# Kernel optimization log

Measured on AMD Instinct MI355X. Metric: run time of the kernel, lower is better.

The kernel has to match this reference:

```python
import jax, jax.numpy as jnp
import numpy as np

N = 100000   # nodes
E = 1600000  # edges (avg degree 16)
F = 128      # num_features
H = 128      # hidden_channels
C = 8        # num_classes


def _gcn_conv(x, src, dst, W, b, num_nodes):
    """PyG GCNConv: add self-loops, symmetric normalization, linear-then-aggregate, +bias."""
    h = x @ W  # [N, out]
    loops = jnp.arange(num_nodes, dtype=src.dtype)
    s = jnp.concatenate([src, loops])
    d = jnp.concatenate([dst, loops])
    deg = jax.ops.segment_sum(jnp.ones_like(s, dtype=h.dtype), d, num_segments=num_nodes)
    dinv = jax.lax.rsqrt(jnp.maximum(deg, 1.0))  # deg >= 1 thanks to self-loops
    norm = dinv[s] * dinv[d]  # [E+N]
    out = jax.ops.segment_sum(h[s] * norm[:, None], d, num_segments=num_nodes)
    return out + b


def setup_inputs() -> dict:
    key = jax.random.key(0)
    k1, k2, k3, k4 = jax.random.split(key, 4)
    x = jax.random.normal(k1, (N, F), dtype=jnp.float32)
    edge_index = jax.random.randint(k2, (2, E), 0, N, dtype=jnp.int32)
    W1 = jax.random.normal(k3, (F, H), dtype=jnp.float32) * (1.0 / np.sqrt(F))
    b1 = jnp.zeros((H,), dtype=jnp.float32)
    W2 = jax.random.normal(k4, (H, C), dtype=jnp.float32) * (1.0 / np.sqrt(H))
    b2 = jnp.zeros((C,), dtype=jnp.float32)
    return {"x": x, "edge_index": edge_index, "W1": W1, "b1": b1, "W2": W2, "b2": b2}


def reference(x, edge_index, W1, b1, W2, b2):
    src, dst = edge_index[0], edge_index[1]
    h = _gcn_conv(x, src, dst, W1, b1, N)
    h = jax.nn.relu(h)
    out = _gcn_conv(h, src, dst, W2, b2, N)
    return out
```

## Files before the change

kernel.cpp:

```cpp
#include <hip/hip_runtime.h>
#include <hip/hip_bf16.h>
#include <hip/hip_fp16.h>

#define NN 100000
#define EE 1600000
#define FF 128
#define HH 128
#define CC 8

#define CH 4096
#define NBK ((NN + 255) / 256)
#define NCH ((EE + CH - 1) / CH)
#define HSZ (NBK * NCH)

typedef _Float16 half8 __attribute__((ext_vector_type(8)));
typedef float f32x4 __attribute__((ext_vector_type(4)));

__global__ __launch_bounds__(1024) void k_scan1(const int* __restrict__ in,
                                                int* __restrict__ outp,
                                                int* __restrict__ bsum, int n) {
  __shared__ int sh[1024];
  int t = threadIdx.x;
  int i = blockIdx.x * 1024 + t;
  int v = (i < n) ? in[i] : 0;
  sh[t] = v;
  __syncthreads();
  for (int offs = 1; offs < 1024; offs <<= 1) {
    int add = (t >= offs) ? sh[t - offs] : 0;
    __syncthreads();
    sh[t] += add;
    __syncthreads();
  }
  if (i < n) outp[i] = sh[t] - v;
  if (t == 1023) bsum[blockIdx.x] = sh[1023];
}

__global__ __launch_bounds__(256) void k_scan2(int* __restrict__ bsum, int nb) {
  __shared__ int sh[256];
  int t = threadIdx.x;
  int v = (t < nb) ? bsum[t] : 0;
  sh[t] = v;
  __syncthreads();
  for (int offs = 1; offs < 256; offs <<= 1) {
    int add = (t >= offs) ? sh[t - offs] : 0;
    __syncthreads();
    sh[t] += add;
    __syncthreads();
  }
  if (t < nb) bsum[t] = sh[t] - v;
}

__global__ __launch_bounds__(1024) void k_scan3(int* __restrict__ outp,
                                                const int* __restrict__ bsum,
                                                int n, int e) {
  int i = blockIdx.x * 1024 + threadIdx.x;
  if (i < n) outp[i] += bsum[blockIdx.x];
  if (i == 0) outp[n] = e;
}

__global__ __launch_bounds__(256) void k_histA(const int* __restrict__ dst,
                                               int* __restrict__ hist) {
  __shared__ int lh[NBK];
  int c = blockIdx.x, t = threadIdx.x;
  for (int b = t; b < NBK; b += 256) lh[b] = 0;
  __syncthreads();
  int e0 = c * CH, e1 = min(e0 + CH, EE);
  for (int j = e0 + t; j < e1; j += 256) atomicAdd(&lh[dst[j] >> 8], 1);
  __syncthreads();
  for (int b = t; b < NBK; b += 256) hist[b * NCH + c] = lh[b];
}

__global__ __launch_bounds__(256) void k_scat_gemm1(
    const int* __restrict__ src, const int* __restrict__ dst,
    const int* __restrict__ hoff, unsigned int* __restrict__ stage,
    const float* __restrict__ x, const float* __restrict__ W,
    __half* __restrict__ h, int n) {
  __shared__ _Float16 Wl[128 * 128];
  int t = threadIdx.x;

  if (blockIdx.x < NCH) {
    int* lcur = (int*)Wl;
    int c = blockIdx.x;
    for (int b = t; b < NBK; b += 256) lcur[b] = hoff[b * NCH + c];
    __syncthreads();
    int e0 = c * CH, e1 = min(e0 + CH, EE);
    for (int j = e0 + t; j < e1; j += 256) {
      int d = dst[j];
      int pos = atomicAdd(&lcur[d >> 8], 1);
      stage[pos] = (unsigned int)src[j] | ((unsigned int)(d & 255) << 17);
    }
    return;
  }

  {
    int c = t & 127;
    int kg0 = t >> 7;
    for (int kg = kg0; kg < 16; kg += 2) {
      _Float16 tmp[8];
#pragma unroll
      for (int j = 0; j < 8; ++j)
        tmp[j] = (_Float16)W[(size_t)(kg * 8 + j) * 128 + c];
      int byteoff = (c * 256 + kg * 16) ^ ((c & 7) << 4);
      *(half8*)((char*)Wl + byteoff) = *(half8*)tmp;
    }
  }
  __syncthreads();

  int row0 = (blockIdx.x - NCH) * 64;
  int w = t >> 6, l = t & 63;
  int rw = w >> 1, cw = w & 1;
  int lr = l & 15, g = l >> 4;

  f32x4 acc[2][4];
#pragma unroll
  for (int ar = 0; ar < 2; ++ar)
#pragma unroll
    for (int bt = 0; bt < 4; ++bt)
#pragma unroll
      for (int r = 0; r < 4; ++r) acc[ar][bt][r] = 0.f;

  for (int kt = 0; kt < 4; ++kt) {
    half8 a[2];
#pragma unroll
    for (int ar = 0; ar < 2; ++ar) {
      int row = row0 + rw * 32 + ar * 16 + lr;
      if (row < n) {
        const float* p = &x[(size_t)row * 128 + kt * 32 + g * 8];
        float4 v0 = *(const float4*)p;
        float4 v1 = *(const float4*)(p + 4);
        a[ar][0] = (_Float16)v0.x; a[ar][1] = (_Float16)v0.y;
        a[ar][2] = (_Float16)v0.z; a[ar][3] = (_Float16)v0.w;
        a[ar][4] = (_Float16)v1.x; a[ar][5] = (_Float16)v1.y;
        a[ar][6] = (_Float16)v1.z; a[ar][7] = (_Float16)v1.w;
      } else {
#pragma unroll
        for (int j = 0; j < 8; ++j) a[ar][j] = (_Float16)0.f;
      }
    }
#pragma unroll
    for (int bt = 0; bt < 4; ++bt) {
      int c = cw * 64 + bt * 16 + lr;
      int byteoff = (c * 256 + kt * 64 + g * 16) ^ ((c & 7) << 4);
      half8 bb = *(const half8*)((const char*)Wl + byteoff);
      acc[0][bt] = __builtin_amdgcn_mfma_f32_16x16x32_f16(a[0], bb, acc[0][bt], 0, 0, 0);
      acc[1][bt] = __builtin_amdgcn_mfma_f32_16x16x32_f16(a[1], bb, acc[1][bt], 0, 0, 0);
    }
  }

#pragma unroll
  for (int ar = 0; ar < 2; ++ar)
#pragma unroll
    for (int bt = 0; bt < 4; ++bt)
#pragma unroll
      for (int r = 0; r < 4; ++r) {
        int row = row0 + rw * 32 + ar * 16 + g * 4 + r;
        int c = cw * 64 + bt * 16 + lr;
        if (row < n) h[(size_t)row * 128 + c] = __float2half(acc[ar][bt][r]);
      }
}

__global__ __launch_bounds__(256) void k_bucketB(const unsigned int* __restrict__ stage,
                                                 const int* __restrict__ hoff,
                                                 int* __restrict__ col,
                                                 int* __restrict__ rowptr,
                                                 float* __restrict__ dinv) {
  __shared__ int lcnt[256];
  __shared__ int lpart[256];
  int b = blockIdx.x, t = threadIdx.x;
  int n0 = b * 256;
  lcnt[t] = 0;
  __syncthreads();
  int e0 = hoff[b * NCH];
  int e1 = hoff[(b + 1) * NCH];
  for (int j = e0 + t; j < e1; j += 256)
    atomicAdd(&lcnt[stage[j] >> 17], 1);
  __syncthreads();
  int c = lcnt[t];
  lpart[t] = c;
  __syncthreads();
  for (int offs = 1; offs < 256; offs <<= 1) {
    int add = (t >= offs) ? lpart[t - offs] : 0;
    __syncthreads();
    lpart[t] += add;
    __syncthreads();
  }
  int base = e0 + lpart[t] - c;
  int node = n0 + t;
  if (node <= NN) rowptr[node] = base;
  if (node < NN) dinv[node] = rsqrtf((float)c + 1.f);
  __syncthreads();
  lcnt[t] = base;
  __syncthreads();
  for (int j = e0 + t; j < e1; j += 256) {
    unsigned int v = stage[j];
    int pos = atomicAdd(&lcnt[v >> 17], 1);
    col[pos] = (int)(v & 0x1FFFFu);
  }
}

__global__ __launch_bounds__(256) void k_agg1(const __half* __restrict__ h,
                                              const int* __restrict__ rowptr,
                                              const int* __restrict__ col,
                                              const float* __restrict__ dinv,
                                              const float* __restrict__ b1,
                                              __half2* __restrict__ out, int n) {
  int wid = threadIdx.x >> 6;
  int lane = threadIdx.x & 63;
  int node = blockIdx.x * 4 + wid;
  if (node >= n) return;
  float dn = dinv[node];
  const __half2* hp = (const __half2*)h;
  float2 acc = make_float2(0.f, 0.f);
  int e0 = rowptr[node], e1 = rowptr[node + 1];
  int e = e0;
  for (; e + 7 < e1; e += 8) {
    int s[8];
#pragma unroll
    for (int u = 0; u < 8; ++u) s[u] = col[e + u];
    float w[8];
    __half2 f[8];
#pragma unroll
    for (int u = 0; u < 8; ++u) w[u] = dinv[s[u]];
#pragma unroll
    for (int u = 0; u < 8; ++u) f[u] = hp[(size_t)s[u] * 64 + lane];
#pragma unroll
    for (int u = 0; u < 8; ++u) {
      float2 ff = __half22float2(f[u]);
      float ww = w[u] * dn;
      acc.x = fmaf(ww, ff.x, acc.x);
      acc.y = fmaf(ww, ff.y, acc.y);
    }
  }
  for (; e + 1 < e1; e += 2) {
    int s0 = col[e], s1 = col[e + 1];
    float w0 = dinv[s0] * dn, w1 = dinv[s1] * dn;
    float2 f0 = __half22float2(hp[(size_t)s0 * 64 + lane]);
    float2 f1 = __half22float2(hp[(size_t)s1 * 64 + lane]);
    acc.x = fmaf(w0, f0.x, acc.x); acc.y = fmaf(w0, f0.y, acc.y);
    acc.x = fmaf(w1, f1.x, acc.x); acc.y = fmaf(w1, f1.y, acc.y);
  }
  if (e < e1) {
    int s = col[e];
    float w = dinv[s] * dn;
    float2 f = __half22float2(hp[(size_t)s * 64 + lane]);
    acc.x = fmaf(w, f.x, acc.x);
    acc.y = fmaf(w, f.y, acc.y);
  }
  {
    float w = dn * dn;
    float2 f = __half22float2(hp[(size_t)node * 64 + lane]);
    acc.x = fmaf(w, f.x, acc.x);
    acc.y = fmaf(w, f.y, acc.y);
  }
  float2 bb = ((const float2*)b1)[lane];
  acc.x = fmaxf(acc.x + bb.x, 0.f);
  acc.y = fmaxf(acc.y + bb.y, 0.f);
  out[(size_t)node * 64 + lane] = __floats2half2_rn(acc.x, acc.y);
}

__global__ __launch_bounds__(256) void k_gemm2(const __half* __restrict__ a,
                                               const float* __restrict__ W2,
                                               __half* __restrict__ h2, int n) {
  int r = blockIdx.x * 256 + threadIdx.x;
  if (r >= n) return;
  float acc[8];
#pragma unroll
  for (int c = 0; c < 8; ++c) acc[c] = 0.f;
  const __half2* ap = (const __half2*)(a + (size_t)r * 128);
#pragma unroll 8
  for (int k2 = 0; k2 < 64; ++k2) {
    float2 v = __half22float2(ap[k2]);
    int k = k2 * 2;
#pragma unroll
    for (int c = 0; c < 8; ++c) {
      acc[c] = fmaf(v.x, W2[(k + 0) * 8 + c], acc[c]);
      acc[c] = fmaf(v.y, W2[(k + 1) * 8 + c], acc[c]);
    }
  }
  union { __half2 h2v[4]; uint4 u; } pk;
#pragma unroll
  for (int c = 0; c < 4; ++c)
    pk.h2v[c] = __floats2half2_rn(acc[2 * c], acc[2 * c + 1]);
  *(uint4*)&h2[(size_t)r * 8] = pk.u;
}

__global__ __launch_bounds__(256) void k_agg2(const __half* __restrict__ h2,
                                              const int* __restrict__ rowptr,
                                              const int* __restrict__ col,
                                              const float* __restrict__ dinv,
                                              const float* __restrict__ b2,
                                              float* __restrict__ out, int n) {
  int gthread = blockIdx.x * 256 + threadIdx.x;
  int node = gthread >> 3, f = gthread & 7;
  if (node >= n) return;
  float dn = dinv[node];
  float acc = 0.f;
  int e0 = rowptr[node], e1 = rowptr[node + 1];
  int e = e0;
  for (; e + 3 < e1; e += 4) {
    int s0 = col[e], s1 = col[e + 1], s2 = col[e + 2], s3 = col[e + 3];
    float w0 = dinv[s0], w1 = dinv[s1], w2 = dinv[s2], w3 = dinv[s3];
    float v0 = __half2float(h2[(size_t)s0 * 8 + f]);
    float v1 = __half2float(h2[(size_t)s1 * 8 + f]);
    float v2 = __half2float(h2[(size_t)s2 * 8 + f]);
    float v3 = __half2float(h2[(size_t)s3 * 8 + f]);
    acc = fmaf(w0 * dn, v0, acc);
    acc = fmaf(w1 * dn, v1, acc);
    acc = fmaf(w2 * dn, v2, acc);
    acc = fmaf(w3 * dn, v3, acc);
  }
  for (; e < e1; ++e) {
    int s = col[e];
    acc = fmaf(dinv[s] * dn, __half2float(h2[(size_t)s * 8 + f]), acc);
  }
  acc = fmaf(dn * dn, __half2float(h2[(size_t)node * 8 + f]), acc);
  out[(size_t)node * 8 + f] = acc + b2[f];
}

extern "C" void kernel_launch(void* const* d_in, const int* in_sizes, int n_in,
                              void* d_out, int out_size, void* d_ws, size_t ws_size,
                              hipStream_t stream) {
  const float* x  = (const float*)d_in[0];
  const int* eidx = (const int*)d_in[1];
  const float* W1 = (const float*)d_in[2];
  const float* b1 = (const float*)d_in[3];
  const float* W2 = (const float*)d_in[4];
  const float* b2 = (const float*)d_in[5];
  float* out = (float*)d_out;
  const int* src = eidx;
  const int* dst = eidx + EE;

  char* ws = (char*)d_ws;
  size_t off = 0;
  auto alloc = [&](size_t bytes) -> char* {
    char* p = ws + off;
    off = (off + bytes + 255) & ~(size_t)255;
    return p;
  };

  float*        dinv   = (float*)       alloc((size_t)NN * 4);
  int*          rowptr = (int*)         alloc((size_t)(NN + 1) * 4);
  int*          bsum   = (int*)         alloc(1024 * 4);
  int*          hist_g = (int*)         alloc((size_t)HSZ * 4);
  int*          hist_s = (int*)         alloc((size_t)(HSZ + 1) * 4);
  unsigned int* stage  = (unsigned int*)alloc((size_t)EE * 4);
  int*          colbuf = (int*)         alloc((size_t)EE * 4);
  __half*       h1     = (__half*)      alloc((size_t)NN * HH * 2);
  __half2*      agg1   = (__half2*)     alloc((size_t)NN * HH * 2);
  __half*       h2     = (__half*)h1;

  int nbScanH = (HSZ + 1023) / 1024;

  k_histA<<<NCH, 256, 0, stream>>>(dst, hist_g);
  k_scan1<<<nbScanH, 1024, 0, stream>>>(hist_g, hist_s, bsum, HSZ);
  k_scan2<<<1, 256, 0, stream>>>(bsum, nbScanH);
  k_scan3<<<nbScanH, 1024, 0, stream>>>(hist_s, bsum, HSZ, EE);

  int nbG1 = (NN + 63) / 64;
  k_scat_gemm1<<<NCH + nbG1, 256, 0, stream>>>(src, dst, hist_s, stage,
                                               x, W1, h1, NN);
  k_bucketB<<<NBK, 256, 0, stream>>>(stage, hist_s, colbuf, rowptr, dinv);

  k_agg1<<<(NN + 3) / 4, 256, 0, stream>>>(h1, rowptr, colbuf, dinv, b1, agg1, NN);
  k_gemm2<<<(NN + 255) / 256, 256, 0, stream>>>((const __half*)agg1, W2, h2, NN);
  k_agg2<<<(NN * 8 + 255) / 256, 256, 0, stream>>>(h2, rowptr, colbuf, dinv,
                                                   b2, out, NN);
}
```

Measured before the change: 165.9 us.

## Fuse second linear layer into aggregation and fold scan offsets into consumers

Merges the layer-2 matmul into the layer-1 aggregation kernel. Each wave stages its aggregated row in shared memory and reduces against W2 with cross-lane shuffles, so the 128-wide intermediate is never written to or re-read from global memory. The scan-add kernel is removed: consumers add the block sums on the fly. The histogram chunk size is doubled to shrink the histogram and scan, and the layer-2 gather loop is unrolled to 8. This removes two launches and a large intermediate buffer, at the cost of some extra shared-memory work and lower parallelism in the scatter phase.

```diff
diff --git a/kernel.cpp b/kernel.cpp
--- a/kernel.cpp
+++ b/kernel.cpp
@@ -8,7 +8,7 @@
 #define HH 128
 #define CC 8
 
-#define CH 4096
+#define CH 8192
 #define NBK ((NN + 255) / 256)
 #define NCH ((EE + CH - 1) / CH)
 #define HSZ (NBK * NCH)
@@ -50,14 +50,6 @@
   if (t < nb) bsum[t] = sh[t] - v;
 }
 
-__global__ __launch_bounds__(1024) void k_scan3(int* __restrict__ outp,
-                                                const int* __restrict__ bsum,
-                                                int n, int e) {
-  int i = blockIdx.x * 1024 + threadIdx.x;
-  if (i < n) outp[i] += bsum[blockIdx.x];
-  if (i == 0) outp[n] = e;
-}
-
 __global__ __launch_bounds__(256) void k_histA(const int* __restrict__ dst,
                                                int* __restrict__ hist) {
   __shared__ int lh[NBK];
@@ -72,7 +64,8 @@
 
 __global__ __launch_bounds__(256) void k_scat_gemm1(
     const int* __restrict__ src, const int* __restrict__ dst,
-    const int* __restrict__ hoff, unsigned int* __restrict__ stage,
+    const int* __restrict__ hist_s, const int* __restrict__ bsum,
+    unsigned int* __restrict__ stage,
     const float* __restrict__ x, const float* __restrict__ W,
     __half* __restrict__ h, int n) {
   __shared__ _Float16 Wl[128 * 128];
@@ -81,7 +74,10 @@
   if (blockIdx.x < NCH) {
     int* lcur = (int*)Wl;
     int c = blockIdx.x;
-    for (int b = t; b < NBK; b += 256) lcur[b] = hoff[b * NCH + c];
+    for (int b = t; b < NBK; b += 256) {
+      int idx = b * NCH + c;
+      lcur[b] = hist_s[idx] + bsum[idx >> 10];
+    }
     __syncthreads();
     int e0 = c * CH, e1 = min(e0 + CH, EE);
     for (int j = e0 + t; j < e1; j += 256) {
@@ -160,7 +156,8 @@
 }
 
 __global__ __launch_bounds__(256) void k_bucketB(const unsigned int* __restrict__ stage,
-                                                 const int* __restrict__ hoff,
+                                                 const int* __restrict__ hist_s,
+                                                 const int* __restrict__ bsum,
                                                  int* __restrict__ col,
                                                  int* __restrict__ rowptr,
                                                  float* __restrict__ dinv) {
@@ -169,9 +166,16 @@
   int b = blockIdx.x, t = threadIdx.x;
   int n0 = b * 256;
   lcnt[t] = 0;
-  __syncthreads();
-  int e0 = hoff[b * NCH];
-  int e1 = hoff[(b + 1) * NCH];
+  int i0 = b * NCH;
+  int e0 = hist_s[i0] + bsum[i0 >> 10];
+  int e1;
+  if (b == NBK - 1) {
+    e1 = EE;
+  } else {
+    int i1 = (b + 1) * NCH;
+    e1 = hist_s[i1] + bsum[i1 >> 10];
+  }
+  __syncthreads();
   for (int j = e0 + t; j < e1; j += 256)
     atomicAdd(&lcnt[stage[j] >> 17], 1);
   __syncthreads();
@@ -198,12 +202,14 @@
   }
 }
 
-__global__ __launch_bounds__(256) void k_agg1(const __half* __restrict__ h,
-                                              const int* __restrict__ rowptr,
-                                              const int* __restrict__ col,
-                                              const float* __restrict__ dinv,
-                                              const float* __restrict__ b1,
-                                              __half2* __restrict__ out, int n) {
+__global__ __launch_bounds__(256) void k_agg1g(const __half* __restrict__ h,
+                                               const int* __restrict__ rowptr,
+                                               const int* __restrict__ col,
+                                               const float* __restrict__ dinv,
+                                               const float* __restrict__ b1,
+                                               const float* __restrict__ W2,
+                                               __half* __restrict__ h2, int n) {
+  __shared__ float arow[4][128];
   int wid = threadIdx.x >> 6;
   int lane = threadIdx.x & 63;
   int node = blockIdx.x * 4 + wid;
@@ -255,33 +261,21 @@
   float2 bb = ((const float2*)b1)[lane];
   acc.x = fmaxf(acc.x + bb.x, 0.f);
   acc.y = fmaxf(acc.y + bb.y, 0.f);
-  out[(size_t)node * 64 + lane] = __floats2half2_rn(acc.x, acc.y);
-}
-
-__global__ __launch_bounds__(256) void k_gemm2(const __half* __restrict__ a,
-                                               const float* __restrict__ W2,
-                                               __half* __restrict__ h2, int n) {
-  int r = blockIdx.x * 256 + threadIdx.x;
-  if (r >= n) return;
-  float acc[8];
-#pragma unroll
-  for (int c = 0; c < 8; ++c) acc[c] = 0.f;
-  const __half2* ap = (const __half2*)(a + (size_t)r * 128);
-#pragma unroll 8
-  for (int k2 = 0; k2 < 64; ++k2) {
-    float2 v = __half22float2(ap[k2]);
-    int k = k2 * 2;
-#pragma unroll
-    for (int c = 0; c < 8; ++c) {
-      acc[c] = fmaf(v.x, W2[(k + 0) * 8 + c], acc[c]);
-      acc[c] = fmaf(v.y, W2[(k + 1) * 8 + c], acc[c]);
-    }
-  }
-  union { __half2 h2v[4]; uint4 u; } pk;
-#pragma unroll
-  for (int c = 0; c < 4; ++c)
-    pk.h2v[c] = __floats2half2_rn(acc[2 * c], acc[2 * c + 1]);
-  *(uint4*)&h2[(size_t)r * 8] = pk.u;
+
+  *(float2*)&arow[wid][2 * lane] = acc;
+  asm volatile("" ::: "memory");
+  int colc = lane & 7;
+  int kg = lane >> 3;
+  float p = 0.f;
+#pragma unroll
+  for (int j = 0; j < 16; ++j) {
+    int k = kg * 16 + j;
+    p = fmaf(arow[wid][k], W2[k * 8 + colc], p);
+  }
+  p += __shfl_xor(p, 8);
+  p += __shfl_xor(p, 16);
+  p += __shfl_xor(p, 32);
+  if (lane < 8) h2[(size_t)node * 8 + colc] = __float2half(p);
 }
 
 __global__ __launch_bounds__(256) void k_agg2(const __half* __restrict__ h2,
@@ -297,17 +291,18 @@
   float acc = 0.f;
   int e0 = rowptr[node], e1 = rowptr[node + 1];
   int e = e0;
-  for (; e + 3 < e1; e += 4) {
-    int s0 = col[e], s1 = col[e + 1], s2 = col[e + 2], s3 = col[e + 3];
-    float w0 = dinv[s0], w1 = dinv[s1], w2 = dinv[s2], w3 = dinv[s3];
-    float v0 = __half2float(h2[(size_t)s0 * 8 + f]);
-    float v1 = __half2float(h2[(size_t)s1 * 8 + f]);
-    float v2 = __half2float(h2[(size_t)s2 * 8 + f]);
-    float v3 = __half2float(h2[(size_t)s3 * 8 + f]);
-    acc = fmaf(w0 * dn, v0, acc);
-    acc = fmaf(w1 * dn, v1, acc);
-    acc = fmaf(w2 * dn, v2, acc);
-    acc = fmaf(w3 * dn, v3, acc);
+  for (; e + 7 < e1; e += 8) {
+    int s[8];
+#pragma unroll
+    for (int u = 0; u < 8; ++u) s[u] = col[e + u];
+    float w[8];
+    float v[8];
+#pragma unroll
+    for (int u = 0; u < 8; ++u) w[u] = dinv[s[u]];
+#pragma unroll
+    for (int u = 0; u < 8; ++u) v[u] = __half2float(h2[(size_t)s[u] * 8 + f]);
+#pragma unroll
+    for (int u = 0; u < 8; ++u) acc = fmaf(w[u] * dn, v[u], acc);
   }
   for (; e < e1; ++e) {
     int s = col[e];
@@ -342,27 +337,25 @@
   int*          rowptr = (int*)         alloc((size_t)(NN + 1) * 4);
   int*          bsum   = (int*)         alloc(1024 * 4);
   int*          hist_g = (int*)         alloc((size_t)HSZ * 4);
-  int*          hist_s = (int*)         alloc((size_t)(HSZ + 1) * 4);
+  int*          hist_s = (int*)         alloc((size_t)HSZ * 4);
   unsigned int* stage  = (unsigned int*)alloc((size_t)EE * 4);
   int*          colbuf = (int*)         alloc((size_t)EE * 4);
   __half*       h1     = (__half*)      alloc((size_t)NN * HH * 2);
-  __half2*      agg1   = (__half2*)     alloc((size_t)NN * HH * 2);
-  __half*       h2     = (__half*)h1;
+  __half*       h2     = (__half*)      alloc((size_t)NN * CC * 2);
 
   int nbScanH = (HSZ + 1023) / 1024;
 
   k_histA<<<NCH, 256, 0, stream>>>(dst, hist_g);
   k_scan1<<<nbScanH, 1024, 0, stream>>>(hist_g, hist_s, bsum, HSZ);
   k_scan2<<<1, 256, 0, stream>>>(bsum, nbScanH);
-  k_scan3<<<nbScanH, 1024, 0, stream>>>(hist_s, bsum, HSZ, EE);
 
   int nbG1 = (NN + 63) / 64;
-  k_scat_gemm1<<<NCH + nbG1, 256, 0, stream>>>(src, dst, hist_s, stage,
+  k_scat_gemm1<<<NCH + nbG1, 256, 0, stream>>>(src, dst, hist_s, bsum, stage,
                                                x, W1, h1, NN);
-  k_bucketB<<<NBK, 256, 0, stream>>>(stage, hist_s, colbuf, rowptr, dinv);
-
-  k_agg1<<<(NN + 3) / 4, 256, 0, stream>>>(h1, rowptr, colbuf, dinv, b1, agg1, NN);
-  k_gemm2<<<(NN + 255) / 256, 256, 0, stream>>>((const __half*)agg1, W2, h2, NN);
+  k_bucketB<<<NBK, 256, 0, stream>>>(stage, hist_s, bsum, colbuf, rowptr, dinv);
+
+  k_agg1g<<<(NN + 3) / 4, 256, 0, stream>>>(h1, rowptr, colbuf, dinv, b1, W2,
+                                            h2, NN);
   k_agg2<<<(NN * 8 + 255) / 256, 256, 0, stream>>>(h2, rowptr, colbuf, dinv,
                                                    b2, out, NN);
 }
```

Result: no change. 165.8 us (-0.0%).
